# Optimization experiments

Measured on AMD Instinct MI355X. Metric: run time of the kernel, lower is better.

The kernel has to match this reference:

```python
import jax, jax.numpy as jnp
import numpy as np

WS = 8          # window_size
POOL = 7        # int(sqrt(agent_num=49)) -> AdaptiveAvgPool1d output size


def _pool_matrix(L, p):
    """Averaging matrix [L, p] replicating torch AdaptiveAvgPool1d(L -> p)."""
    starts = np.floor(np.arange(p) * L / p).astype(int)
    ends = np.ceil((np.arange(p) + 1) * L / p).astype(int)
    P = np.zeros((L, p), dtype=np.float32)
    for i in range(p):
        P[starts[i]:ends[i], i] = 1.0 / (ends[i] - starts[i])
    return jnp.asarray(P)


def setup_inputs() -> dict:
    key = jax.random.key(0)
    ks = jax.random.split(key, 4)
    B, C, H, W = 8, 96, 192, 192
    s = 1.0 / np.sqrt(C)
    return {
        "x": jax.random.normal(ks[0], (B, C, H, W), jnp.float32),
        "Wv": jax.random.normal(ks[1], (C, C), jnp.float32) * s,
        "bv": jnp.zeros((C,), jnp.float32),
        "Wq": jax.random.normal(ks[2], (C, C), jnp.float32) * s,
        "bq": jnp.zeros((C,), jnp.float32),
        "Wk": jax.random.normal(ks[3], (C, C), jnp.float32) * s,
        "bk": jnp.zeros((C,), jnp.float32),
    }


def _conv1x1(x, Wt, b):
    # Conv2d(dim, dim, 1): weight [out, in]
    return jnp.einsum('bchw,oc->bohw', x, Wt) + b[None, :, None, None]


def reference(x, Wv, bv, Wq, bq, Wk, bk):
    B, C, H, W = x.shape
    ws = WS
    nh, nw = H // ws, W // ws
    L = ws * ws  # tokens per window (64)

    v = _conv1x1(x, Wv, bv)
    q = _conv1x1(x, Wq, bq)
    k = _conv1x1(x, Wk, bk)

    def win(t):  # b c (h dh) (w dw) -> (b h w) (dh dw) c
        t = t.reshape(B, C, nh, ws, nw, ws)
        return t.transpose(0, 2, 4, 3, 5, 1).reshape(B * nh * nw, L, C)

    vw, qw, kw = win(v), win(q), win(k)  # (N, 64, C) each

    # agent tokens: adaptive avg pool over the 64 in-window positions -> 7
    P = _pool_matrix(L, POOL)
    agent = jnp.einsum('nlc,lp->npc', qw, P)  # (N, 7, C)

    # agent attention (attn_drop = 0 -> identity)
    a_attn = jax.nn.softmax(jnp.einsum('npc,nlc->npl', agent, kw), axis=-1)
    agent_v = jnp.einsum('npl,nlc->npc', a_attn, vw)            # (N, 7, C)
    q_attn = jax.nn.softmax(jnp.einsum('nlc,npc->nlp', qw, agent), axis=-1)
    f = jnp.einsum('nlp,npc->nlc', q_attn, agent_v)             # (N, 64, C)

    # (b h w) (dh dw) c -> b c (h dh) (w dw)
    out = f.reshape(B, nh, nw, ws, ws, C).transpose(0, 5, 1, 3, 2, 4)
    return out.reshape(B, C, H, W)
```

## Files before the change

kernel.cpp:

```cpp
#include <hip/hip_runtime.h>


constexpr int C_   = 96;
constexpr int Wimg = 192;
constexpr int HWp  = 192 * 192;
constexpr int NWIN = 24;
constexpr int Pp   = 7;

typedef __attribute__((ext_vector_type(8))) __bf16 bf16x8;
typedef __attribute__((ext_vector_type(4))) __bf16 bf16x4;
typedef __attribute__((ext_vector_type(8))) short  short8;
typedef __attribute__((ext_vector_type(4))) float  f32x4;
union frag_u { short8 s; bf16x8 b; };

constexpr int XWS   = 0;
constexpr int RA    = 12288;
constexpr int XPH   = RA;
constexpr int XPL   = RA + 1600;
constexpr int LRAW  = RA;
constexpr int RB    = 16512;
constexpr int GKQH  = RB;
constexpr int GKQL  = RB + 3200;
constexpr int AVH   = RB;
constexpr int AVL   = RB + 1536;
constexpr int QATH  = 22912;
constexpr int QATL  = 23936;
constexpr int BIAS  = 24960;
constexpr int SMEMB = 25024;

constexpr int WS_FRAG_BYTE = 18944 * 4;
constexpr int WS_WV_BYTE   = WS_FRAG_BYTE + 84 * 1024;


__device__ __forceinline__ void bar() {
    asm volatile("s_waitcnt lgkmcnt(0)" ::: "memory");
    __builtin_amdgcn_s_barrier();
}

__device__ __forceinline__ short8 xws_fragA(const unsigned char* S, int mt, int ks, int lane) {
    const int c  = mt * 16 + (lane & 15);
    const int l2 = ks * 64 + ((lane >> 4) << 4);
    return *reinterpret_cast<const short8*>(S + XWS + c * 128 + (l2 ^ ((c & 7) << 4)));
}

__device__ __forceinline__ void pack_hilo4(unsigned char* S, int hi_off, int lo_off,
                                           const f32x4 acc) {
    bf16x4 h, l;
    #pragma unroll
    for (int i = 0; i < 4; ++i) {
        h[i] = (__bf16)acc[i];
        l[i] = (__bf16)(acc[i] - (float)h[i]);
    }
    *reinterpret_cast<bf16x4*>(S + hi_off) = h;
    *reinterpret_cast<bf16x4*>(S + lo_off) = l;
}


__global__ void precompute_mats(const float* __restrict__ Wq,
                                const float* __restrict__ Wk,
                                float* __restrict__ Mk,
                                float* __restrict__ Mq)
{
    const int c  = blockIdx.x;
    const int cp = threadIdx.x;
    float ak = 0.f, aq = 0.f;
    for (int a = 0; a < C_; ++a) {
        const float wq = Wq[a * C_ + c];
        ak = fmaf(wq, Wk[a * C_ + cp], ak);
        aq = fmaf(wq, Wq[a * C_ + cp], aq);
    }
    Mk[c * C_ + cp] = ak;
    Mq[c * C_ + cp] = aq;
}

__global__ void precompute_vecs(const float* __restrict__ Wq,
                                const float* __restrict__ Wk,
                                const float* __restrict__ bq,
                                const float* __restrict__ bk,
                                float* __restrict__ uk,  float* __restrict__ uq,
                                float* __restrict__ bk2, float* __restrict__ bq2,
                                float* __restrict__ scal)
{
    const int c = threadIdx.x;
    float a_uk = 0.f, a_uq = 0.f, a_bk2 = 0.f, a_bq2 = 0.f;
    for (int a = 0; a < C_; ++a) {
        const float wqc = Wq[a * C_ + c];
        a_uk  = fmaf(wqc, bk[a], a_uk);
        a_uq  = fmaf(wqc, bq[a], a_uq);
        a_bk2 = fmaf(bq[a], Wk[a * C_ + c], a_bk2);
        a_bq2 = fmaf(bq[a], Wq[a * C_ + c], a_bq2);
    }
    uk[c] = a_uk; uq[c] = a_uq; bk2[c] = a_bk2; bq2[c] = a_bq2;
    if (c == 0) {
        float sk = 0.f, sq = 0.f;
        for (int a = 0; a < C_; ++a) { sk += bq[a] * bk[a]; sq += bq[a] * bq[a]; }
        scal[0] = sk; scal[1] = sq;
    }
}

__global__ void precompute_frags(const float* __restrict__ ws,
                                 const float* __restrict__ Wv,
                                 unsigned char* __restrict__ wsb)
{
    const int bid = blockIdx.x, lane = threadIdx.x;
    short8 o;
    if (bid < 84) {
        const int hl = bid & 1, ks = (bid >> 1) % 3, nt = (bid / 6) % 7, mat = bid / 42;
        const float* M = ws + (mat ? 9216 : 0);
        const float* u = ws + (mat ? 18528 : 18432);
        const int col = nt * 16 + (lane & 15);
        #pragma unroll
        for (int j = 0; j < 8; ++j) {
            const int k = ks * 32 + (lane >> 4) * 8 + j;
            const float raw = (col < 96) ? M[k * 96 + col] : ((col == 96) ? u[k] : 0.f);
            const __bf16 hi = (__bf16)raw;
            union { __bf16 h; short s; } cv;
            cv.h = hl ? (__bf16)(raw - (float)hi) : hi;
            o[j] = cv.s;
        }
        *reinterpret_cast<short8*>(wsb + WS_FRAG_BYTE + bid * 1024 + lane * 16) = o;
    } else {
        const int wb = bid - 84;
        const int hl = wb & 1, ks = (wb >> 1) % 3, mt = wb / 6;
        const int row = mt * 16 + (lane & 15);
        #pragma unroll
        for (int j = 0; j < 8; ++j) {
            const int c = ks * 32 + (lane >> 4) * 8 + j;
            const float raw = Wv[row * 96 + c];
            const __bf16 hi = (__bf16)raw;
            union { __bf16 h; short s; } cv;
            cv.h = hl ? (__bf16)(raw - (float)hi) : hi;
            o[j] = cv.s;
        }
        *reinterpret_cast<short8*>(wsb + WS_WV_BYTE + wb * 1024 + lane * 16) = o;
    }
}

#define LOADPAIR(dstH, dstL, tab, slot_h) do {                                               \
    (dstH).s = *reinterpret_cast<const short8*>((tab) + (slot_h) * 1024 + (lane << 4));      \
    (dstL).s = *reinterpret_cast<const short8*>((tab) + ((slot_h) + 1) * 1024 + (lane << 4));\
} while (0)


__global__ __launch_bounds__(256, 5) void camixer_main(
    const float* __restrict__ x,
    const float* __restrict__ bv,
    const float* __restrict__ bk2,
    const float* __restrict__ bq2,
    const float* __restrict__ scal,
    const unsigned char* __restrict__ mfrag,
    const unsigned char* __restrict__ wvfrag,
    float* __restrict__ out)
{
    __shared__ __align__(16) unsigned char S[SMEMB];
    float* Lraw   = (float*)(S + LRAW);
    float* bias16 = (float*)(S + BIAS);

    const int t = threadIdx.x;
    const int lane = t & 63, w = t >> 6;
    const int wid = ((blockIdx.x & 7) * 576) + (blockIdx.x >> 3);
    const int b  = wid / (NWIN * NWIN);
    const int r  = wid % (NWIN * NWIN);
    const int h0 = (r / NWIN) * 8;
    const int w0 = (r % NWIN) * 8;
    const int base = b * C_ * HWp + h0 * Wimg + w0;
    const float scal0 = scal[0], scal1 = scal[1];
    const short8 zero8 = {0, 0, 0, 0, 0, 0, 0, 0};

    frag_u B0h[3], B0l[3];
    LOADPAIR(B0h[0], B0l[0], mfrag, (w * 3 + 0) * 2);
    LOADPAIR(B0h[1], B0l[1], mfrag, (w * 3 + 1) * 2);
    LOADPAIR(B0h[2], B0l[2], mfrag, (w * 3 + 2) * 2);

    {
        const float4* x4 = reinterpret_cast<const float4*>(x);
        #pragma unroll
        for (int rr = 0; rr < 2; ++rr) {
            const int idx = t + (rr << 8);
            if (idx < 384) {
                const int dw4 = idx & 1;
                const int dh  = (idx >> 1) & 7;
                const int c4  = idx >> 4;
                const int c0 = c4 * 4, l0 = dh * 8 + dw4 * 4;
                #pragma unroll
                for (int j = 0; j < 4; ++j) {
                    const int c = c0 + j;
                    const float4 v = x4[(base + c * HWp + dh * Wimg + dw4 * 4) >> 2];
                    bf16x4 d = {(__bf16)v.x, (__bf16)v.y, (__bf16)v.z, (__bf16)v.w};
                    *reinterpret_cast<bf16x4*>(S + XWS + c * 128 + ((l0 * 2) ^ ((c & 7) << 4))) = d;
                }
            }
        }
    }
    bar();

    {
        frag_u PBh[2], PBl[2];
        {
            const int p = lane & 15;
            const __bf16 PH = (__bf16)0.1f;
            const __bf16 PL = (__bf16)(0.1f - (float)PH);
            const int sp = (p < 7) ? ((p << 6) / 7) : 1000;
            #pragma unroll
            for (int ks = 0; ks < 2; ++ks)
                #pragma unroll
                for (int j = 0; j < 8; ++j) {
                    const int l = ks * 32 + (lane >> 4) * 8 + j;
                    const bool in = (l >= sp) && (l < sp + 10);
                    PBh[ks].b[j] = in ? PH : (__bf16)0.f;
                    PBl[ks].b[j] = in ? PL : (__bf16)0.f;
                }
        }
        #pragma unroll
        for (int rnd = 0; rnd < 2; ++rnd) {
            const int mt = rnd ? (4 + w) : w;
            if (rnd == 0 || w < 2) {
                f32x4 acc = {0.f, 0.f, 0.f, 0.f};
                #pragma unroll
                for (int ks = 0; ks < 2; ++ks) {
                    frag_u A;
                    A.s = xws_fragA(S, mt, ks, lane);
                    acc = __builtin_amdgcn_mfma_f32_16x16x32_bf16(A.b, PBh[ks].b, acc, 0, 0, 0);
                    acc = __builtin_amdgcn_mfma_f32_16x16x32_bf16(A.b, PBl[ks].b, acc, 0, 0, 0);
                }
                const int p = lane & 15;
                if (p < 8) {
                    const int c0 = mt * 16 + (lane >> 4) * 4;
                    pack_hilo4(S, XPH + p * 200 + c0 * 2, XPL + p * 200 + c0 * 2, acc);
                }
            }
        }
    }
    bar();

    {
        frag_u Bh[3], Bl[3];
        #pragma unroll
        for (int ks = 0; ks < 3; ++ks) {
            const int off = ((lane & 15) & 7) * 200 + (ks * 32 + (lane >> 4) * 8) * 2;
            Bh[ks].s = *reinterpret_cast<const short8*>(S + XPH + off);
            Bl[ks].s = *reinterpret_cast<const short8*>(S + XPL + off);
        }

        #define G0TILE(TT, AH, AL) do {                                               \
            const int tt_ = (TT);                                                     \
            const int mat_ = (tt_ >= 7) ? 1 : 0;                                      \
            const int nt_  = tt_ - 7 * mat_;                             \
            f32x4 acc = {0.f, 0.f, 0.f, 0.f};                                         \
            acc = __builtin_amdgcn_mfma_f32_16x16x32_bf16(AH[0].b, Bh[0].b, acc, 0,0,0); \
            acc = __builtin_amdgcn_mfma_f32_16x16x32_bf16(AL[0].b, Bh[0].b, acc, 0,0,0); \
            acc = __builtin_amdgcn_mfma_f32_16x16x32_bf16(AH[0].b, Bl[0].b, acc, 0,0,0); \
            acc = __builtin_amdgcn_mfma_f32_16x16x32_bf16(AH[1].b, Bh[1].b, acc, 0,0,0); \
            acc = __builtin_amdgcn_mfma_f32_16x16x32_bf16(AL[1].b, Bh[1].b, acc, 0,0,0); \
            acc = __builtin_amdgcn_mfma_f32_16x16x32_bf16(AH[1].b, Bl[1].b, acc, 0,0,0); \
            acc = __builtin_amdgcn_mfma_f32_16x16x32_bf16(AH[2].b, Bh[2].b, acc, 0,0,0); \
            acc = __builtin_amdgcn_mfma_f32_16x16x32_bf16(AL[2].b, Bh[2].b, acc, 0,0,0); \
            acc = __builtin_amdgcn_mfma_f32_16x16x32_bf16(AH[2].b, Bl[2].b, acc, 0,0,0); \
            const int p_ = lane & 15;                                    \
            if (nt_ < 6) {                                                            \
                if (p_ < 8) {                                                         \
                    const int cp0_ = nt_ * 16 + (lane >> 4) * 4;                      \
                    const float4 b4_ = *reinterpret_cast<const float4*>(              \
                        (mat_ ? bq2 : bk2) + cp0_);                                   \
                    f32x4 av_;                                                        \
                    av_[0] = acc[0] + b4_.x; av_[1] = acc[1] + b4_.y;                 \
                    av_[2] = acc[2] + b4_.z; av_[3] = acc[3] + b4_.w;                 \
                    const int pr_ = p_ + 8 * mat_;                                    \
                    pack_hilo4(S, GKQH + pr_ * 200 + cp0_ * 2,                        \
                               GKQL + pr_ * 200 + cp0_ * 2, av_);                     \
                }                                                                     \
            } else if ((lane >> 4) == 0 && p_ < 8) {                                  \
                bias16[p_ + 8 * mat_] = acc[0];             \
            }                                                                         \
        } while (0)

        frag_u B1h[3], B1l[3], B2h[3], B2l[3], B3h[3], B3l[3];
        LOADPAIR(B1h[0], B1l[0], mfrag, ((w + 4) * 3 + 0) * 2);
        LOADPAIR(B1h[1], B1l[1], mfrag, ((w + 4) * 3 + 1) * 2);
        LOADPAIR(B1h[2], B1l[2], mfrag, ((w + 4) * 3 + 2) * 2);
        G0TILE(w, B0h, B0l);
        LOADPAIR(B2h[0], B2l[0], mfrag, ((w + 8) * 3 + 0) * 2);
        LOADPAIR(B2h[1], B2l[1], mfrag, ((w + 8) * 3 + 1) * 2);
        LOADPAIR(B2h[2], B2l[2], mfrag, ((w + 8) * 3 + 2) * 2);
        G0TILE(w + 4, B1h, B1l);
        if (w < 2) {
            LOADPAIR(B3h[0], B3l[0], mfrag, ((w + 12) * 3 + 0) * 2);
            LOADPAIR(B3h[1], B3l[1], mfrag, ((w + 12) * 3 + 1) * 2);
            LOADPAIR(B3h[2], B3l[2], mfrag, ((w + 12) * 3 + 2) * 2);
        }
        G0TILE(w + 8, B2h, B2l);
        if (w < 2) G0TILE(w + 12, B3h, B3l);
        #undef G0TILE
    }
    bar();

    {
        frag_u B[3];
        {
            const int l2 = (w * 16 + (lane & 15)) * 2;
            const int kb = (lane >> 4) << 10;
            #pragma unroll
            for (int j = 0; j < 8; ++j) {
                const int aj = kb + j * 128 + (l2 ^ (j << 4));
                B[0].b[j] = *reinterpret_cast<const __bf16*>(S + XWS + aj);
                B[1].b[j] = *reinterpret_cast<const __bf16*>(S + XWS + 4096 + aj);
                B[2].b[j] = *reinterpret_cast<const __bf16*>(S + XWS + 8192 + aj);
            }
        }
        frag_u Ah[3], Al[3];
        #pragma unroll
        for (int ks = 0; ks < 3; ++ks) {
            const int off = (lane & 15) * 200 + (ks * 32 + (lane >> 4) * 8) * 2;
            Ah[ks].s = *reinterpret_cast<const short8*>(S + GKQH + off);
            Al[ks].s = *reinterpret_cast<const short8*>(S + GKQL + off);
        }
        f32x4 acc = {0.f, 0.f, 0.f, 0.f};
        #pragma unroll
        for (int ks = 0; ks < 3; ++ks) {
            acc = __builtin_amdgcn_mfma_f32_16x16x32_bf16(Ah[ks].b, B[ks].b, acc, 0, 0, 0);
            acc = __builtin_amdgcn_mfma_f32_16x16x32_bf16(Al[ks].b, B[ks].b, acc, 0, 0, 0);
        }
        const int colL = w * 16 + (lane & 15);
        #pragma unroll
        for (int rr = 0; rr < 4; ++rr) {
            const int pr = (lane >> 4) * 4 + rr;
            Lraw[pr * 66 + colL] = acc[rr] + bias16[pr] + (pr < 8 ? scal0 : scal1);
        }
    }
    bar();

    if (w < 3) {
        #pragma unroll
        for (int rr = 0; rr < 2; ++rr) {
            const int pp = w + 3 * rr;
            const float v = Lraw[pp * 66 + lane];
            float mx = v;
            #pragma unroll
            for (int off = 32; off; off >>= 1) mx = fmaxf(mx, __shfl_xor(mx, off));
            const float e = __expf(v - mx);
            float s = e;
            #pragma unroll
            for (int off = 32; off; off >>= 1) s += __shfl_xor(s, off);
            const float a = e / s;
            const __bf16 hb = (__bf16)a;
            const __bf16 lb = (__bf16)(a - (float)hb);
            const int ks = lane >> 5;
            const int off_b = ((pp + 16 * ((lane >> 3) & 3)) << 4) + ((lane & 7) << 1);
            *reinterpret_cast<__bf16*>(S + RB + (ks << 10) + off_b) = hb;
            *reinterpret_cast<__bf16*>(S + RB + ((2 + ks) << 10) + off_b) = lb;
        }
    } else {
        {
            const int pp = 6;
            const float v = Lraw[pp * 66 + lane];
            float mx = v;
            #pragma unroll
            for (int off = 32; off; off >>= 1) mx = fmaxf(mx, __shfl_xor(mx, off));
            const float e = __expf(v - mx);
            float s = e;
            #pragma unroll
            for (int off = 32; off; off >>= 1) s += __shfl_xor(s, off);
            const float a = e / s;
            const __bf16 hb = (__bf16)a;
            const __bf16 lb = (__bf16)(a - (float)hb);
            const int ks = lane >> 5;
            const int off_b = ((pp + 16 * ((lane >> 3) & 3)) << 4) + ((lane & 7) << 1);
            *reinterpret_cast<__bf16*>(S + RB + (ks << 10) + off_b) = hb;
            *reinterpret_cast<__bf16*>(S + RB + ((2 + ks) << 10) + off_b) = lb;
        }
        float vv[Pp];
        float mx = -1e30f;
        #pragma unroll
        for (int p = 0; p < Pp; ++p) { vv[p] = Lraw[(8 + p) * 66 + lane]; mx = fmaxf(mx, vv[p]); }
        float s = 0.f;
        #pragma unroll
        for (int p = 0; p < Pp; ++p) { vv[p] = __expf(vv[p] - mx); s += vv[p]; }
        const float inv = 1.f / s;
        frag_u qh, ql;
        #pragma unroll
        for (int p = 0; p < 8; ++p) {
            const float a = (p < Pp) ? vv[p] * inv : 0.f;
            const __bf16 hb = (__bf16)a;
            qh.b[p] = hb;
            ql.b[p] = (__bf16)(a - (float)hb);
        }
        *reinterpret_cast<short8*>(S + QATH + lane * 16) = qh.s;
        *reinterpret_cast<short8*>(S + QATL + lane * 16) = ql.s;
    }
    bar();

    frag_u V0h[3], V0l[3], V1h[3], V1l[3];
    {
        LOADPAIR(V0h[0], V0l[0], wvfrag, (w * 3 + 0) * 2);
        LOADPAIR(V0h[1], V0l[1], wvfrag, (w * 3 + 1) * 2);
        LOADPAIR(V0h[2], V0l[2], wvfrag, (w * 3 + 2) * 2);
        if (w < 2) {
            LOADPAIR(V1h[0], V1l[0], wvfrag, ((4 + w) * 3 + 0) * 2);
            LOADPAIR(V1h[1], V1l[1], wvfrag, ((4 + w) * 3 + 1) * 2);
            LOADPAIR(V1h[2], V1l[2], wvfrag, ((4 + w) * 3 + 2) * 2);
        }

        frag_u Bh[2], Bl[2];
        #pragma unroll
        for (int ks = 0; ks < 2; ++ks) {
            Bh[ks].s = *reinterpret_cast<const short8*>(S + RB + (ks << 10) + (lane << 4));
            Bl[ks].s = *reinterpret_cast<const short8*>(S + RB + ((2 + ks) << 10) + (lane << 4));
        }
        const int mt0 = (w < 2) ? w * 2 : (w + 2);
        const int nmt = (w < 2) ? 2 : 1;
        for (int m = 0; m < nmt; ++m) {
            const int mt = mt0 + m;
            f32x4 acc = {0.f, 0.f, 0.f, 0.f};
            #pragma unroll
            for (int ks = 0; ks < 2; ++ks) {
                frag_u A;
                A.s = xws_fragA(S, mt, ks, lane);
                acc = __builtin_amdgcn_mfma_f32_16x16x32_bf16(A.b, Bh[ks].b, acc, 0, 0, 0);
                acc = __builtin_amdgcn_mfma_f32_16x16x32_bf16(A.b, Bl[ks].b, acc, 0, 0, 0);
            }
            const int p = lane & 15;
            if (p < 8) {
                const int c0 = mt * 16 + (lane >> 4) * 4;
                pack_hilo4(S, XPH + p * 200 + c0 * 2, XPL + p * 200 + c0 * 2, acc);
            }
        }
    }
    bar();

    {
        const bool row7 = ((lane & 15) & 7) == 7;
        frag_u Ah[3], Al[3];
        #pragma unroll
        for (int ks = 0; ks < 3; ++ks) {
            const int off = ((lane & 15) & 7) * 200 + (ks * 32 + (lane >> 4) * 8) * 2;
            Ah[ks].s = row7 ? zero8 : *reinterpret_cast<const short8*>(S + XPH + off);
            Al[ks].s = row7 ? zero8 : *reinterpret_cast<const short8*>(S + XPL + off);
        }
        #define G3TILE(OT, VH, VL) do {                     \
            f32x4 acc = {0.f, 0.f, 0.f, 0.f};                                         \
            acc = __builtin_amdgcn_mfma_f32_16x16x32_bf16(Ah[0].b, VH[0].b, acc, 0,0,0); \
            acc = __builtin_amdgcn_mfma_f32_16x16x32_bf16(Al[0].b, VH[0].b, acc, 0,0,0); \
            acc = __builtin_amdgcn_mfma_f32_16x16x32_bf16(Ah[0].b, VL[0].b, acc, 0,0,0); \
            acc = __builtin_amdgcn_mfma_f32_16x16x32_bf16(Ah[1].b, VH[1].b, acc, 0,0,0); \
            acc = __builtin_amdgcn_mfma_f32_16x16x32_bf16(Al[1].b, VH[1].b, acc, 0,0,0); \
            acc = __builtin_amdgcn_mfma_f32_16x16x32_bf16(Ah[1].b, VL[1].b, acc, 0,0,0); \
            acc = __builtin_amdgcn_mfma_f32_16x16x32_bf16(Ah[2].b, VH[2].b, acc, 0,0,0); \
            acc = __builtin_amdgcn_mfma_f32_16x16x32_bf16(Al[2].b, VH[2].b, acc, 0,0,0); \
            acc = __builtin_amdgcn_mfma_f32_16x16x32_bf16(Ah[2].b, VL[2].b, acc, 0,0,0); \
            if ((lane >> 4) < 2) {                    \
                const int o_ = (OT) * 16 + (lane & 15);                               \
                const float bvo_ = bv[o_];                                            \
                f32x4 av_;                                                            \
                av_[0] = acc[0] + bvo_; av_[1] = acc[1] + bvo_;                       \
                av_[2] = acc[2] + bvo_; av_[3] = acc[3] + bvo_;                       \
                const int p0_ = (lane >> 4) * 4;                                      \
                pack_hilo4(S, AVH + o_ * 16 + p0_ * 2, AVL + o_ * 16 + p0_ * 2, av_); \
            }                                                                         \
        } while (0)
        G3TILE(w, V0h, V0l);
        if (w < 2) G3TILE(4 + w, V1h, V1l);
        #undef G3TILE
    }
    bar();

    {
        const int kblk = lane >> 4, nlow = lane & 15;
        const int l = w * 16 + nlow;
        frag_u Bh, Bl;
        if (kblk == 0) {
            Bh.s = *reinterpret_cast<const short8*>(S + QATH + l * 16);
            Bl.s = *reinterpret_cast<const short8*>(S + QATL + l * 16);
        } else { Bh.s = zero8; Bl.s = zero8; }
        const int obase = b * C_ * HWp + (h0 + (l >> 3)) * Wimg + w0 + (l & 7);
        #pragma unroll
        for (int mt = 0; mt < 6; ++mt) {
            frag_u Ah, Al;
            if (kblk == 0) {
                Ah.s = *reinterpret_cast<const short8*>(S + AVH + (mt * 16 + nlow) * 16);
                Al.s = *reinterpret_cast<const short8*>(S + AVL + (mt * 16 + nlow) * 16);
            } else { Ah.s = zero8; Al.s = zero8; }
            f32x4 acc = {0.f, 0.f, 0.f, 0.f};
            acc = __builtin_amdgcn_mfma_f32_16x16x32_bf16(Ah.b, Bh.b, acc, 0, 0, 0);
            acc = __builtin_amdgcn_mfma_f32_16x16x32_bf16(Ah.b, Bl.b, acc, 0, 0, 0);
            acc = __builtin_amdgcn_mfma_f32_16x16x32_bf16(Al.b, Bh.b, acc, 0, 0, 0);
            #pragma unroll
            for (int rr = 0; rr < 4; ++rr) {
                const int o = mt * 16 + kblk * 4 + rr;
                out[obase + o * HWp] = acc[rr];
            }
        }
    }
}


extern "C" void kernel_launch(void* const* d_in, const int* in_sizes, int n_in,
                              void* d_out, int out_size, void* d_ws, size_t ws_size,
                              hipStream_t stream)
{
    const float* x  = (const float*)d_in[0];
    const float* Wv = (const float*)d_in[1];
    const float* bv = (const float*)d_in[2];
    const float* Wq = (const float*)d_in[3];
    const float* bq = (const float*)d_in[4];
    const float* Wk = (const float*)d_in[5];
    const float* bk = (const float*)d_in[6];
    float* out = (float*)d_out;

    float* ws = (float*)d_ws;
    float* Mk   = ws;
    float* Mq   = ws + 9216;
    float* uk   = ws + 18432;
    float* uq   = ws + 18528;
    float* bk2  = ws + 18624;
    float* bq2  = ws + 18720;
    float* scal = ws + 18816;
    unsigned char* wsb = (unsigned char*)d_ws;

    hipLaunchKernelGGL(precompute_mats, dim3(C_), dim3(C_), 0, stream,
                       Wq, Wk, Mk, Mq);
    hipLaunchKernelGGL(precompute_vecs, dim3(1), dim3(C_), 0, stream,
                       Wq, Wk, bq, bk, uk, uq, bk2, bq2, scal);
    hipLaunchKernelGGL(precompute_frags, dim3(120), dim3(64), 0, stream,
                       ws, Wv, wsb);
    hipLaunchKernelGGL(camixer_main, dim3(8 * NWIN * NWIN), dim3(256), 0, stream,
                       x, bv, bk2, bq2, scal,
                       wsb + WS_FRAG_BYTE, wsb + WS_WV_BYTE, out);
}
```

Baseline: 74.16 us.

## Merge precompute kernels and fuse query-side softmax into MFMA epilogue

The two small precompute kernels become one launch with 97 blocks: block 96 computes the bias vectors and the other blocks compute the matrix products. In the main kernel, the per-token softmax over the 7 agent logits now runs directly on the MFMA accumulators, using lane shuffles across the two 16-lane groups. This drops the round trip through LDS for those rows and balances the remaining agent-side softmax work across waves. It saves one kernel launch and some LDS traffic and serial work, at the cost of more complex per-lane epilogue logic.

```diff
diff --git a/kernel.cpp b/kernel.cpp
--- a/kernel.cpp
+++ b/kernel.cpp
@@ -56,45 +56,43 @@
 }
 
 
-__global__ void precompute_mats(const float* __restrict__ Wq,
-                                const float* __restrict__ Wk,
-                                float* __restrict__ Mk,
-                                float* __restrict__ Mq)
+__global__ void precompute_mv(const float* __restrict__ Wq,
+                              const float* __restrict__ Wk,
+                              const float* __restrict__ bq,
+                              const float* __restrict__ bk,
+                              float* __restrict__ Mk,  float* __restrict__ Mq,
+                              float* __restrict__ uk,  float* __restrict__ uq,
+                              float* __restrict__ bk2, float* __restrict__ bq2,
+                              float* __restrict__ scal)
 {
-    const int c  = blockIdx.x;
-    const int cp = threadIdx.x;
-    float ak = 0.f, aq = 0.f;
-    for (int a = 0; a < C_; ++a) {
-        const float wq = Wq[a * C_ + c];
-        ak = fmaf(wq, Wk[a * C_ + cp], ak);
-        aq = fmaf(wq, Wq[a * C_ + cp], aq);
-    }
-    Mk[c * C_ + cp] = ak;
-    Mq[c * C_ + cp] = aq;
-}
-
-__global__ void precompute_vecs(const float* __restrict__ Wq,
-                                const float* __restrict__ Wk,
-                                const float* __restrict__ bq,
-                                const float* __restrict__ bk,
-                                float* __restrict__ uk,  float* __restrict__ uq,
-                                float* __restrict__ bk2, float* __restrict__ bq2,
-                                float* __restrict__ scal)
-{
-    const int c = threadIdx.x;
-    float a_uk = 0.f, a_uq = 0.f, a_bk2 = 0.f, a_bq2 = 0.f;
-    for (int a = 0; a < C_; ++a) {
-        const float wqc = Wq[a * C_ + c];
-        a_uk  = fmaf(wqc, bk[a], a_uk);
-        a_uq  = fmaf(wqc, bq[a], a_uq);
-        a_bk2 = fmaf(bq[a], Wk[a * C_ + c], a_bk2);
-        a_bq2 = fmaf(bq[a], Wq[a * C_ + c], a_bq2);
-    }
-    uk[c] = a_uk; uq[c] = a_uq; bk2[c] = a_bk2; bq2[c] = a_bq2;
-    if (c == 0) {
-        float sk = 0.f, sq = 0.f;
-        for (int a = 0; a < C_; ++a) { sk += bq[a] * bk[a]; sq += bq[a] * bq[a]; }
-        scal[0] = sk; scal[1] = sq;
+    const int bid = blockIdx.x;
+    if (bid < 96) {
+        const int c  = bid;
+        const int cp = threadIdx.x;
+        float ak = 0.f, aq = 0.f;
+        for (int a = 0; a < C_; ++a) {
+            const float wq = Wq[a * C_ + c];
+            ak = fmaf(wq, Wk[a * C_ + cp], ak);
+            aq = fmaf(wq, Wq[a * C_ + cp], aq);
+        }
+        Mk[c * C_ + cp] = ak;
+        Mq[c * C_ + cp] = aq;
+    } else {
+        const int c = threadIdx.x;
+        float a_uk = 0.f, a_uq = 0.f, a_bk2 = 0.f, a_bq2 = 0.f;
+        for (int a = 0; a < C_; ++a) {
+            const float wqc = Wq[a * C_ + c];
+            a_uk  = fmaf(wqc, bk[a], a_uk);
+            a_uq  = fmaf(wqc, bq[a], a_uq);
+            a_bk2 = fmaf(bq[a], Wk[a * C_ + c], a_bk2);
+            a_bq2 = fmaf(bq[a], Wq[a * C_ + c], a_bq2);
+        }
+        uk[c] = a_uk; uq[c] = a_uq; bk2[c] = a_bk2; bq2[c] = a_bq2;
+        if (c == 0) {
+            float sk = 0.f, sq = 0.f;
+            for (int a = 0; a < C_; ++a) { sk += bq[a] * bk[a]; sq += bq[a] * bq[a]; }
+            scal[0] = sk; scal[1] = sq;
+        }
     }
 }
 
@@ -321,71 +319,75 @@
             acc = __builtin_amdgcn_mfma_f32_16x16x32_bf16(Al[ks].b, B[ks].b, acc, 0, 0, 0);
         }
         const int colL = w * 16 + (lane & 15);
-        #pragma unroll
-        for (int rr = 0; rr < 4; ++rr) {
-            const int pr = (lane >> 4) * 4 + rr;
-            Lraw[pr * 66 + colL] = acc[rr] + bias16[pr] + (pr < 8 ? scal0 : scal1);
-        }
-    }
-    bar();
-
-    if (w < 3) {
+        const int g = lane >> 4;
+        if (g < 2) {
+            #pragma unroll
+            for (int rr = 0; rr < 4; ++rr) {
+                const int pr = g * 4 + rr;
+                Lraw[pr * 66 + colL] = acc[rr] + bias16[pr] + scal0;
+            }
+        } else {
+            const bool isg3 = (g == 3);
+            float v[4];
+            #pragma unroll
+            for (int rr = 0; rr < 4; ++rr)
+                v[rr] = acc[rr] + bias16[8 + (g - 2) * 4 + rr] + scal1;
+            float mymax = fmaxf(fmaxf(v[0], v[1]), isg3 ? v[2] : fmaxf(v[2], v[3]));
+            const float omax = __shfl_xor(mymax, 16);
+            const float mx = fmaxf(mymax, omax);
+            float e[4];
+            e[0] = __expf(v[0] - mx); e[1] = __expf(v[1] - mx); e[2] = __expf(v[2] - mx);
+            e[3] = isg3 ? 0.f : __expf(v[3] - mx);
+            float mysum = (e[0] + e[1]) + (e[2] + e[3]);
+            const float osum = __shfl_xor(mysum, 16);
+            const float inv = 1.f / (mysum + osum);
+            float a[4], pa[4];
+            #pragma unroll
+            for (int rr = 0; rr < 4; ++rr) a[rr] = e[rr] * inv;
+            #pragma unroll
+            for (int rr = 0; rr < 4; ++rr) pa[rr] = __shfl_xor(a[rr], 16);
+            if (!isg3) {
+                frag_u qh, ql;
+                #pragma unroll
+                for (int p = 0; p < 4; ++p) {
+                    const __bf16 hb = (__bf16)a[p];
+                    qh.b[p] = hb; ql.b[p] = (__bf16)(a[p] - (float)hb);
+                }
+                #pragma unroll
+                for (int p = 0; p < 4; ++p) {
+                    const __bf16 hb = (__bf16)pa[p];
+                    qh.b[4 + p] = hb; ql.b[4 + p] = (__bf16)(pa[p] - (float)hb);
+                }
+                *reinterpret_cast<short8*>(S + QATH + colL * 16) = qh.s;
+                *reinterpret_cast<short8*>(S + QATL + colL * 16) = ql.s;
+            }
+        }
+    }
+    bar();
+
+    {
+        const int nrows = (w < 3) ? 2 : 1;
         #pragma unroll
         for (int rr = 0; rr < 2; ++rr) {
-            const int pp = w + 3 * rr;
-            const float v = Lraw[pp * 66 + lane];
-            float mx = v;
-            #pragma unroll
-            for (int off = 32; off; off >>= 1) mx = fmaxf(mx, __shfl_xor(mx, off));
-            const float e = __expf(v - mx);
-            float s = e;
-            #pragma unroll
-            for (int off = 32; off; off >>= 1) s += __shfl_xor(s, off);
-            const float a = e / s;
-            const __bf16 hb = (__bf16)a;
-            const __bf16 lb = (__bf16)(a - (float)hb);
-            const int ks = lane >> 5;
-            const int off_b = ((pp + 16 * ((lane >> 3) & 3)) << 4) + ((lane & 7) << 1);
-            *reinterpret_cast<__bf16*>(S + RB + (ks << 10) + off_b) = hb;
-            *reinterpret_cast<__bf16*>(S + RB + ((2 + ks) << 10) + off_b) = lb;
-        }
-    } else {
-        {
-            const int pp = 6;
-            const float v = Lraw[pp * 66 + lane];
-            float mx = v;
-            #pragma unroll
-            for (int off = 32; off; off >>= 1) mx = fmaxf(mx, __shfl_xor(mx, off));
-            const float e = __expf(v - mx);
-            float s = e;
-            #pragma unroll
-            for (int off = 32; off; off >>= 1) s += __shfl_xor(s, off);
-            const float a = e / s;
-            const __bf16 hb = (__bf16)a;
-            const __bf16 lb = (__bf16)(a - (float)hb);
-            const int ks = lane >> 5;
-            const int off_b = ((pp + 16 * ((lane >> 3) & 3)) << 4) + ((lane & 7) << 1);
-            *reinterpret_cast<__bf16*>(S + RB + (ks << 10) + off_b) = hb;
-            *reinterpret_cast<__bf16*>(S + RB + ((2 + ks) << 10) + off_b) = lb;
-        }
-        float vv[Pp];
-        float mx = -1e30f;
-        #pragma unroll
-        for (int p = 0; p < Pp; ++p) { vv[p] = Lraw[(8 + p) * 66 + lane]; mx = fmaxf(mx, vv[p]); }
-        float s = 0.f;
-        #pragma unroll
-        for (int p = 0; p < Pp; ++p) { vv[p] = __expf(vv[p] - mx); s += vv[p]; }
-        const float inv = 1.f / s;
-        frag_u qh, ql;
-        #pragma unroll
-        for (int p = 0; p < 8; ++p) {
-            const float a = (p < Pp) ? vv[p] * inv : 0.f;
-            const __bf16 hb = (__bf16)a;
-            qh.b[p] = hb;
-            ql.b[p] = (__bf16)(a - (float)hb);
-        }
-        *reinterpret_cast<short8*>(S + QATH + lane * 16) = qh.s;
-        *reinterpret_cast<short8*>(S + QATL + lane * 16) = ql.s;
+            if (rr < nrows) {
+                const int pp = (w < 3) ? (w + 3 * rr) : 6;
+                const float v = Lraw[pp * 66 + lane];
+                float mx = v;
+                #pragma unroll
+                for (int off = 32; off; off >>= 1) mx = fmaxf(mx, __shfl_xor(mx, off));
+                const float e = __expf(v - mx);
+                float s = e;
+                #pragma unroll
+                for (int off = 32; off; off >>= 1) s += __shfl_xor(s, off);
+                const float a = e / s;
+                const __bf16 hb = (__bf16)a;
+                const __bf16 lb = (__bf16)(a - (float)hb);
+                const int ks = lane >> 5;
+                const int off_b = ((pp + 16 * ((lane >> 3) & 3)) << 4) + ((lane & 7) << 1);
+                *reinterpret_cast<__bf16*>(S + RB + (ks << 10) + off_b) = hb;
+                *reinterpret_cast<__bf16*>(S + RB + ((2 + ks) << 10) + off_b) = lb;
+            }
+        }
     }
     bar();
 
@@ -516,10 +518,8 @@
     float* scal = ws + 18816;
     unsigned char* wsb = (unsigned char*)d_ws;
 
-    hipLaunchKernelGGL(precompute_mats, dim3(C_), dim3(C_), 0, stream,
-                       Wq, Wk, Mk, Mq);
-    hipLaunchKernelGGL(precompute_vecs, dim3(1), dim3(C_), 0, stream,
-                       Wq, Wk, bq, bk, uk, uq, bk2, bq2, scal);
+    hipLaunchKernelGGL(precompute_mv, dim3(97), dim3(C_), 0, stream,
+                       Wq, Wk, bq, bk, Mk, Mq, uk, uq, bk2, bq2, scal);
     hipLaunchKernelGGL(precompute_frags, dim3(120), dim3(64), 0, stream,
                        ws, Wv, wsb);
     hipLaunchKernelGGL(camixer_main, dim3(8 * NWIN * NWIN), dim3(256), 0, stream,
```

Measured after the change: 72.12 us. 1.03x faster.
